# Kernel optimization log

Hardware: AMD Instinct MI355X
Metric: run time of the kernel (lower is better)

Reference implementation:

```python
import jax, jax.numpy as jnp
import numpy as np

GRID = (160, 160, 160)
RADIUS_FACTOR = 3.0
PATCH = 20      # fixed patch edge; covers ceil(c+r)-floor(c-r)+1 for r <= 9 voxels
CHUNK = 500
N_POINTS = 25000


def _quat_to_rot(q):
    # normalized quaternion -> rotation matrix (matches torch reference)
    q = q / jnp.clip(jnp.linalg.norm(q, axis=-1, keepdims=True), 1e-6)
    w, x, y, z = q[..., 0], q[..., 1], q[..., 2], q[..., 3]
    ww, xx, yy, zz = w * w, x * x, y * y, z * z
    wx, wy, wz = w * x, w * y, w * z
    xy, xz, yz = x * y, x * z, y * z
    r0 = jnp.stack([ww + xx - yy - zz, 2 * (xy - wz), 2 * (xz + wy)], -1)
    r1 = jnp.stack([2 * (xy + wz), ww - xx + yy - zz, 2 * (yz - wx)], -1)
    r2 = jnp.stack([2 * (xz - wy), 2 * (yz + wx), ww - xx - yy + zz], -1)
    return jnp.stack([r0, r1, r2], -2)


def setup_inputs():
    key = jax.random.key(0)
    k1, k2, k3, k4 = jax.random.split(key, 4)
    centers = jax.random.uniform(k1, (N_POINTS, 3), dtype=jnp.float32)
    # scales in [1.5, 3.0] voxels -> patch radius = 3*max(scale) <= 9 < PATCH/2
    log_scales = jnp.log(jax.random.uniform(k2, (N_POINTS, 3), minval=1.5, maxval=3.0, dtype=jnp.float32))
    quats = jax.random.normal(k3, (N_POINTS, 4), dtype=jnp.float32)
    rho = 0.1 * jax.random.normal(k4, (N_POINTS, 2), dtype=jnp.float32)  # (real, imag)
    return {"centers": centers, "log_scales": log_scales, "quats": quats, "rho": rho}


def _splat(centers, log_scales, quats, rho):
    D, H, W = GRID
    span = jnp.array([D - 1, H - 1, W - 1], jnp.float32)
    scales = jnp.exp(log_scales)                                  # [N,3]
    R = _quat_to_rot(quats)                                       # [N,3,3]
    inv = 1.0 / jnp.clip(scales, 1e-4) ** 2                       # diag of S^-2
    prec = jnp.einsum('nij,nj,nkj->nik', R, inv, R)               # R diag R^T, [N,3,3]
    cv = centers * span                                           # voxel-space centers
    rad = jnp.max(scales, axis=-1) * RADIUS_FACTOR                # per-point patch radius
    base = jnp.floor(cv - rad[:, None]).astype(jnp.int32)         # zmin/ymin/xmin (pre-clip)
    hi = jnp.ceil(cv + rad[:, None]).astype(jnp.int32)            # zmax/ymax/xmax (pre-clip)
    amp_mag = jnp.sqrt(rho[:, 0] ** 2 + rho[:, 1] ** 2)
    valid = (amp_mag >= 1e-6) & (rad >= 1e-3)                     # torch skip conditions
    dims = jnp.array([D, H, W], jnp.int32)

    nchunk = N_POINTS // CHUNK
    ck = lambda a: a.reshape((nchunk, CHUNK) + a.shape[1:])
    xs = (ck(cv), ck(base), ck(hi), ck(prec), ck(rho), ck(valid))
    offs = jnp.arange(PATCH, dtype=jnp.int32)

    def step(vol, x):
        cv_c, base_c, hi_c, p, rho_c, val_c = x
        idx = base_c[:, :, None] + offs                           # [C,3,P] voxel indices
        d = idx.astype(jnp.float32) - cv_c[:, :, None]            # [C,3,P] rel coords
        m = (idx >= 0) & (idx < dims[None, :, None]) & (idx <= hi_c[:, :, None])
        dz, dy, dx = d[:, 0], d[:, 1], d[:, 2]                    # [C,P] each
        # exponent = rel^T prec rel, built separably (prec is symmetric)
        e = ((p[:, 0, 0, None] * dz * dz)[:, :, None, None]
             + (p[:, 1, 1, None] * dy * dy)[:, None, :, None]
             + (p[:, 2, 2, None] * dx * dx)[:, None, None, :]
             + (2.0 * p[:, 0, 1, None, None] * dz[:, :, None] * dy[:, None, :])[:, :, :, None]
             + (2.0 * p[:, 0, 2, None, None] * dz[:, :, None] * dx[:, None, :])[:, :, None, :]
             + (2.0 * p[:, 1, 2, None, None] * dy[:, :, None] * dx[:, None, :])[:, None, :, :])
        w = jnp.exp(-0.5 * e)                                     # [C,P,P,P]
        mask = (m[:, 0, :, None, None] & m[:, 1, None, :, None] & m[:, 2, None, None, :]
                & val_c[:, None, None, None])
        w = jnp.where(mask, w, 0.0)
        iz = jnp.clip(idx[:, 0], 0, D - 1)
        iy = jnp.clip(idx[:, 1], 0, H - 1)
        ix = jnp.clip(idx[:, 2], 0, W - 1)
        lin = (iz[:, :, None, None] * H + iy[:, None, :, None]) * W + ix[:, None, None, :]
        contrib = w[..., None] * rho_c[:, None, None, None, :]    # [C,P,P,P,2] (re,im)
        vol = vol.at[lin.reshape(-1)].add(contrib.reshape(-1, 2))
        return vol, None

    vol, _ = jax.lax.scan(step, jnp.zeros((D * H * W, 2), jnp.float32), xs)
    return vol.reshape(D, H, W, 2)


def reference(centers, log_scales, quats, rho):
    return _splat(centers, log_scales, quats, rho)
```

## Files before the change

kernel.cpp:

```cpp
#include <hip/hip_runtime.h>


namespace {
constexpr int GD = 160, GH = 160, GW = 160;
constexpr int NPTS = 25000;
constexpr int PATCH = 20;
constexpr int TS  = 8;
constexpr int TPD = GD / TS;
constexpr int NT  = TPD * TPD * TPD;
constexpr int CAP = 384;
constexpr int PSTRIDE = 16;
constexpr float L2E = 1.4426950408889634f;
}


__global__ __launch_bounds__(256) void prep_bin(
    const float* __restrict__ centers,
    const float* __restrict__ log_scales,
    const float* __restrict__ quats,
    const float* __restrict__ rho,
    float* __restrict__ params,
    int* __restrict__ counts,
    unsigned short* __restrict__ list)
{
    const int t = blockIdx.x * 256 + threadIdx.x;
    const int gid  = t >> 6;
    const int lane = t & 63;

    const float r0 = rho[gid * 2 + 0];
    const float r1 = rho[gid * 2 + 1];
    const float s0 = __expf(log_scales[gid * 3 + 0]);
    const float s1 = __expf(log_scales[gid * 3 + 1]);
    const float s2 = __expf(log_scales[gid * 3 + 2]);

    const float smax = fmaxf(s0, fmaxf(s1, s2));
    const float rad  = smax * 3.0f;
    const float amp2 = r0 * r0 + r1 * r1;

    const float cvz = centers[gid * 3 + 0] * (float)(GD - 1);
    const float cvy = centers[gid * 3 + 1] * (float)(GH - 1);
    const float cvx = centers[gid * 3 + 2] * (float)(GW - 1);

    const int bz = (int)floorf(cvz - rad);
    const int by = (int)floorf(cvy - rad);
    const int bx = (int)floorf(cvx - rad);
    const int hz = (int)ceilf(cvz + rad);
    const int hy = (int)ceilf(cvy + rad);
    const int hx = (int)ceilf(cvx + rad);

    const int loz = max(bz, 0), upz = min(min(hz, GD - 1), bz + PATCH - 1);
    const int loy = max(by, 0), upy = min(min(hy, GH - 1), by + PATCH - 1);
    const int lox = max(bx, 0), upx = min(min(hx, GW - 1), bx + PATCH - 1);

    const bool valid = (amp2 >= 1e-12f) && (rad >= 1e-3f) &&
                       (upz >= loz) && (upy >= loy) && (upx >= lox);

    const float q0 = quats[gid * 4 + 0], q1 = quats[gid * 4 + 1];
    const float q2 = quats[gid * 4 + 2], q3 = quats[gid * 4 + 3];
    float qn = sqrtf(q0 * q0 + q1 * q1 + q2 * q2 + q3 * q3);
    qn = fmaxf(qn, 1e-6f);
    const float w = q0 / qn, x = q1 / qn, y = q2 / qn, z = q3 / qn;

    const float R00 = w * w + x * x - y * y - z * z;
    const float R01 = 2.f * (x * y - w * z);
    const float R02 = 2.f * (x * z + w * y);
    const float R10 = 2.f * (x * y + w * z);
    const float R11 = w * w - x * x + y * y - z * z;
    const float R12 = 2.f * (y * z - w * x);
    const float R20 = 2.f * (x * z - w * y);
    const float R21 = 2.f * (y * z + w * x);
    const float R22 = w * w - x * x - y * y + z * z;

    const float c0 = fmaxf(s0, 1e-4f); const float i0 = 1.f / (c0 * c0);
    const float c1 = fmaxf(s1, 1e-4f); const float i1 = 1.f / (c1 * c1);
    const float c2 = fmaxf(s2, 1e-4f); const float i2 = 1.f / (c2 * c2);

    const float p00 = R00 * R00 * i0 + R01 * R01 * i1 + R02 * R02 * i2;
    const float p01 = R00 * R10 * i0 + R01 * R11 * i1 + R02 * R12 * i2;
    const float p02 = R00 * R20 * i0 + R01 * R21 * i1 + R02 * R22 * i2;
    const float p11 = R10 * R10 * i0 + R11 * R11 * i1 + R12 * R12 * i2;
    const float p12 = R10 * R20 * i0 + R11 * R21 * i1 + R12 * R22 * i2;
    const float p22 = R20 * R20 * i0 + R21 * R21 * i1 + R22 * R22 * i2;

    const float q00s = -0.5f * L2E * p00;
    const float v    = __builtin_amdgcn_exp2f(2.f * q00s);

    const int zl = valid ? loz : 255, zu = valid ? upz : 0;
    const int yl = valid ? loy : 255, yu = valid ? upy : 0;
    const int xl = valid ? lox : 255, xu = valid ? upx : 0;
    const int loPack = zl | (yl << 8) | (xl << 16) | (zu << 24);
    const int upPack = yu | (xu << 8);

    if (lane == 0) {
        float4* P = reinterpret_cast<float4*>(params + (size_t)gid * PSTRIDE);
        P[0] = make_float4(q00s, -L2E * p01, -L2E * p02, -0.5f * L2E * p11);
        P[1] = make_float4(-L2E * p12, -0.5f * L2E * p22, cvz, cvy);
        P[2] = make_float4(cvx, r0, r1, __int_as_float(loPack));
        P[3] = make_float4(__int_as_float(upPack), v, 0.f, 0.f);
    }

    if (!valid) return;

    const int tz0 = loz >> 3, tz1 = upz >> 3;
    const int ty0 = loy >> 3, ty1 = upy >> 3;
    const int tx0 = lox >> 3, tx1 = upx >> 3;
    const int tz = tz0 + (lane >> 4);
    const int ty = ty0 + ((lane >> 2) & 3);
    const int tx = tx0 + (lane & 3);
    if (tz > tz1 || ty > ty1 || tx > tx1) return;
    const int tile = (tz * TPD + ty) * TPD + tx;
    const int pos = atomicAdd(&counts[tile], 1);
    if (pos < CAP) list[(size_t)tile * CAP + pos] = (unsigned short)gid;
}

__global__ __launch_bounds__(256) void gather(
    const float* __restrict__ params,
    const int* __restrict__ counts,
    const unsigned short* __restrict__ list,
    float2* __restrict__ out)
{
    const int wli  = threadIdx.x >> 6;
    const int tile = __builtin_amdgcn_readfirstlane(blockIdx.x * 4 + wli);
    const int tz = tile / (TPD * TPD);
    const int rem = tile - tz * (TPD * TPD);
    const int ty = rem / TPD;
    const int tx = rem - ty * TPD;

    const int lane = threadIdx.x & 63;
    const int ly = lane >> 3, lx = lane & 7;
    const int iy = ty * TS + ly;
    const int ix = tx * TS + lx;
    const int z0 = tz * TS;
    const float fy = (float)iy, fx = (float)ix, fz = (float)z0;

    int cnt = counts[tile];
    if (cnt > CAP) cnt = CAP;
    const float4* p4 = reinterpret_cast<const float4*>(params);
    const unsigned short* tl = list + (size_t)tile * CAP;

    float ar[8], ai[8];
#pragma unroll
    for (int i = 0; i < 8; ++i) { ar[i] = 0.f; ai[i] = 0.f; }

    for (int g = 0; g < cnt; ++g) {
        const int gid = __builtin_amdgcn_readfirstlane((int)tl[g]);
        const float4 Pa = p4[(size_t)gid * 4 + 0];
        const float4 Pb = p4[(size_t)gid * 4 + 1];
        const float4 Pc = p4[(size_t)gid * 4 + 2];
        const float4 Pd = p4[(size_t)gid * 4 + 3];
        const int lo = __float_as_int(Pc.w);
        const int up = __float_as_int(Pd.x);
        const int loy_ = (lo >> 8) & 255, lox_ = (lo >> 16) & 255;
        const int upy_ = up & 255,        upx_ = (up >> 8) & 255;
        if (iy < loy_ || iy > upy_ || ix < lox_ || ix > upx_) continue;
        const int zl = (lo & 255) - z0;
        const int zu = ((lo >> 24) & 255) - z0;

        const float dy = fy - Pb.w;
        const float dx = fx - Pc.x;
        const float C = fmaf(dy, fmaf(Pa.w, dy, Pb.x * dx), Pb.y * dx * dx);
        const float B = fmaf(Pa.y, dy, Pa.z * dx);
        const float dz = fz - Pb.z;
        const float t0 = fmaf(dz, fmaf(Pa.x, dz, B), C);
        const float dt = fmaf(Pa.x, fmaf(2.f, dz, 1.f), B);
        float wgt = __builtin_amdgcn_exp2f(t0);
        float u   = __builtin_amdgcn_exp2f(dt);
        const float v = Pd.y;
        const float r0 = Pc.y, r1 = Pc.z;
#pragma unroll
        for (int i = 0; i < 8; ++i) {
            const float wm = (i >= zl && i <= zu) ? wgt : 0.f;
            ar[i] = fmaf(wm, r0, ar[i]);
            ai[i] = fmaf(wm, r1, ai[i]);
            wgt *= u;
            u *= v;
        }
    }

#pragma unroll
    for (int i = 0; i < 8; ++i)
        out[((size_t)(z0 + i) * GH + iy) * GW + ix] = make_float2(ar[i], ai[i]);
}

extern "C" void kernel_launch(void* const* d_in, const int* in_sizes, int n_in,
                              void* d_out, int out_size, void* d_ws, size_t ws_size,
                              hipStream_t stream) {
    const float* centers    = (const float*)d_in[0];
    const float* log_scales = (const float*)d_in[1];
    const float* quats      = (const float*)d_in[2];
    const float* rho        = (const float*)d_in[3];

    float* params = (float*)d_ws;
    int* counts = (int*)(params + (size_t)NPTS * PSTRIDE);
    unsigned short* list = (unsigned short*)(counts + NT);

    hipMemsetAsync(counts, 0, NT * sizeof(int), stream);
    prep_bin<<<(NPTS * 64) / 256, 256, 0, stream>>>(centers, log_scales, quats,
                                                    rho, params, counts, list);
    gather<<<NT / 4, 256, 0, stream>>>(params, counts, list, (float2*)d_out);
}
```

Before: 191.8 us.

## Fuse memset, binning and gather into one cooperative persistent kernel

Replaces the memset plus two kernel launches with a single cooperative kernel. It zeroes the counts, computes per-point parameters and bins them serially per thread, then gathers per tile, with grid-wide syncs between phases. In the gather phase each wave stages batches of 16 point parameter records in LDS instead of issuing scalar global loads per point. Lane masking is made branchless. The aim is to remove launch gaps and per-point global load latency, at the cost of grid.sync overhead, persistent-grid occupancy limits, and serial atomic loops per point in the binning phase.

New measurement: 377.9 us. 97.0% more time.

```diff
diff --git a/kernel.cpp b/kernel.cpp
--- a/kernel.cpp
+++ b/kernel.cpp
@@ -1,4 +1,7 @@
 #include <hip/hip_runtime.h>
+#include <hip/hip_cooperative_groups.h>
+
+namespace cg = cooperative_groups;
 
 
 namespace {
@@ -14,172 +17,183 @@
 }
 
 
-__global__ __launch_bounds__(256) void prep_bin(
+__global__ __launch_bounds__(256, 8) void fused(
     const float* __restrict__ centers,
     const float* __restrict__ log_scales,
     const float* __restrict__ quats,
     const float* __restrict__ rho,
     float* __restrict__ params,
     int* __restrict__ counts,
-    unsigned short* __restrict__ list)
+    unsigned short* __restrict__ list,
+    float2* __restrict__ out)
 {
-    const int t = blockIdx.x * 256 + threadIdx.x;
-    const int gid  = t >> 6;
-    const int lane = t & 63;
-
-    const float r0 = rho[gid * 2 + 0];
-    const float r1 = rho[gid * 2 + 1];
-    const float s0 = __expf(log_scales[gid * 3 + 0]);
-    const float s1 = __expf(log_scales[gid * 3 + 1]);
-    const float s2 = __expf(log_scales[gid * 3 + 2]);
-
-    const float smax = fmaxf(s0, fmaxf(s1, s2));
-    const float rad  = smax * 3.0f;
-    const float amp2 = r0 * r0 + r1 * r1;
-
-    const float cvz = centers[gid * 3 + 0] * (float)(GD - 1);
-    const float cvy = centers[gid * 3 + 1] * (float)(GH - 1);
-    const float cvx = centers[gid * 3 + 2] * (float)(GW - 1);
-
-    const int bz = (int)floorf(cvz - rad);
-    const int by = (int)floorf(cvy - rad);
-    const int bx = (int)floorf(cvx - rad);
-    const int hz = (int)ceilf(cvz + rad);
-    const int hy = (int)ceilf(cvy + rad);
-    const int hx = (int)ceilf(cvx + rad);
-
-    const int loz = max(bz, 0), upz = min(min(hz, GD - 1), bz + PATCH - 1);
-    const int loy = max(by, 0), upy = min(min(hy, GH - 1), by + PATCH - 1);
-    const int lox = max(bx, 0), upx = min(min(hx, GW - 1), bx + PATCH - 1);
-
-    const bool valid = (amp2 >= 1e-12f) && (rad >= 1e-3f) &&
-                       (upz >= loz) && (upy >= loy) && (upx >= lox);
-
-    const float q0 = quats[gid * 4 + 0], q1 = quats[gid * 4 + 1];
-    const float q2 = quats[gid * 4 + 2], q3 = quats[gid * 4 + 3];
-    float qn = sqrtf(q0 * q0 + q1 * q1 + q2 * q2 + q3 * q3);
-    qn = fmaxf(qn, 1e-6f);
-    const float w = q0 / qn, x = q1 / qn, y = q2 / qn, z = q3 / qn;
-
-    const float R00 = w * w + x * x - y * y - z * z;
-    const float R01 = 2.f * (x * y - w * z);
-    const float R02 = 2.f * (x * z + w * y);
-    const float R10 = 2.f * (x * y + w * z);
-    const float R11 = w * w - x * x + y * y - z * z;
-    const float R12 = 2.f * (y * z - w * x);
-    const float R20 = 2.f * (x * z - w * y);
-    const float R21 = 2.f * (y * z + w * x);
-    const float R22 = w * w - x * x - y * y + z * z;
-
-    const float c0 = fmaxf(s0, 1e-4f); const float i0 = 1.f / (c0 * c0);
-    const float c1 = fmaxf(s1, 1e-4f); const float i1 = 1.f / (c1 * c1);
-    const float c2 = fmaxf(s2, 1e-4f); const float i2 = 1.f / (c2 * c2);
-
-    const float p00 = R00 * R00 * i0 + R01 * R01 * i1 + R02 * R02 * i2;
-    const float p01 = R00 * R10 * i0 + R01 * R11 * i1 + R02 * R12 * i2;
-    const float p02 = R00 * R20 * i0 + R01 * R21 * i1 + R02 * R22 * i2;
-    const float p11 = R10 * R10 * i0 + R11 * R11 * i1 + R12 * R12 * i2;
-    const float p12 = R10 * R20 * i0 + R11 * R21 * i1 + R12 * R22 * i2;
-    const float p22 = R20 * R20 * i0 + R21 * R21 * i1 + R22 * R22 * i2;
-
-    const float q00s = -0.5f * L2E * p00;
-    const float v    = __builtin_amdgcn_exp2f(2.f * q00s);
-
-    const int zl = valid ? loz : 255, zu = valid ? upz : 0;
-    const int yl = valid ? loy : 255, yu = valid ? upy : 0;
-    const int xl = valid ? lox : 255, xu = valid ? upx : 0;
-    const int loPack = zl | (yl << 8) | (xl << 16) | (zu << 24);
-    const int upPack = yu | (xu << 8);
-
-    if (lane == 0) {
+    cg::grid_group grid = cg::this_grid();
+    const int nthreads = (int)gridDim.x * 256;
+    const int tid = blockIdx.x * 256 + threadIdx.x;
+
+    for (int i = tid; i < NT; i += nthreads) counts[i] = 0;
+    grid.sync();
+
+    for (int gid = tid; gid < NPTS; gid += nthreads) {
+        const float r0 = rho[gid * 2 + 0];
+        const float r1 = rho[gid * 2 + 1];
+        const float s0 = __expf(log_scales[gid * 3 + 0]);
+        const float s1 = __expf(log_scales[gid * 3 + 1]);
+        const float s2 = __expf(log_scales[gid * 3 + 2]);
+
+        const float smax = fmaxf(s0, fmaxf(s1, s2));
+        const float rad  = smax * 3.0f;
+        const float amp2 = r0 * r0 + r1 * r1;
+
+        const float cvz = centers[gid * 3 + 0] * (float)(GD - 1);
+        const float cvy = centers[gid * 3 + 1] * (float)(GH - 1);
+        const float cvx = centers[gid * 3 + 2] * (float)(GW - 1);
+
+        const int bz = (int)floorf(cvz - rad);
+        const int by = (int)floorf(cvy - rad);
+        const int bx = (int)floorf(cvx - rad);
+        const int hz = (int)ceilf(cvz + rad);
+        const int hy = (int)ceilf(cvy + rad);
+        const int hx = (int)ceilf(cvx + rad);
+
+        const int loz = max(bz, 0), upz = min(min(hz, GD - 1), bz + PATCH - 1);
+        const int loy = max(by, 0), upy = min(min(hy, GH - 1), by + PATCH - 1);
+        const int lox = max(bx, 0), upx = min(min(hx, GW - 1), bx + PATCH - 1);
+
+        const bool valid = (amp2 >= 1e-12f) && (rad >= 1e-3f) &&
+                           (upz >= loz) && (upy >= loy) && (upx >= lox);
+
+        const float q0 = quats[gid * 4 + 0], q1 = quats[gid * 4 + 1];
+        const float q2 = quats[gid * 4 + 2], q3 = quats[gid * 4 + 3];
+        float qn = sqrtf(q0 * q0 + q1 * q1 + q2 * q2 + q3 * q3);
+        qn = fmaxf(qn, 1e-6f);
+        const float w = q0 / qn, x = q1 / qn, y = q2 / qn, z = q3 / qn;
+
+        const float R00 = w * w + x * x - y * y - z * z;
+        const float R01 = 2.f * (x * y - w * z);
+        const float R02 = 2.f * (x * z + w * y);
+        const float R10 = 2.f * (x * y + w * z);
+        const float R11 = w * w - x * x + y * y - z * z;
+        const float R12 = 2.f * (y * z - w * x);
+        const float R20 = 2.f * (x * z - w * y);
+        const float R21 = 2.f * (y * z + w * x);
+        const float R22 = w * w - x * x - y * y + z * z;
+
+        const float c0 = fmaxf(s0, 1e-4f); const float i0 = 1.f / (c0 * c0);
+        const float c1 = fmaxf(s1, 1e-4f); const float i1 = 1.f / (c1 * c1);
+        const float c2 = fmaxf(s2, 1e-4f); const float i2 = 1.f / (c2 * c2);
+
+        const float p00 = R00 * R00 * i0 + R01 * R01 * i1 + R02 * R02 * i2;
+        const float p01 = R00 * R10 * i0 + R01 * R11 * i1 + R02 * R12 * i2;
+        const float p02 = R00 * R20 * i0 + R01 * R21 * i1 + R02 * R22 * i2;
+        const float p11 = R10 * R10 * i0 + R11 * R11 * i1 + R12 * R12 * i2;
+        const float p12 = R10 * R20 * i0 + R11 * R21 * i1 + R12 * R22 * i2;
+        const float p22 = R20 * R20 * i0 + R21 * R21 * i1 + R22 * R22 * i2;
+
+        const float q00s = -0.5f * L2E * p00;
+        const float v    = __builtin_amdgcn_exp2f(2.f * q00s);
+
+        const int zl = valid ? loz : 255, zu = valid ? upz : 0;
+        const int yl = valid ? loy : 255, yu = valid ? upy : 0;
+        const int xl = valid ? lox : 255, xu = valid ? upx : 0;
+        const int loPack = zl | (yl << 8) | (xl << 16) | (zu << 24);
+        const int upPack = yu | (xu << 8);
+
         float4* P = reinterpret_cast<float4*>(params + (size_t)gid * PSTRIDE);
         P[0] = make_float4(q00s, -L2E * p01, -L2E * p02, -0.5f * L2E * p11);
         P[1] = make_float4(-L2E * p12, -0.5f * L2E * p22, cvz, cvy);
         P[2] = make_float4(cvx, r0, r1, __int_as_float(loPack));
         P[3] = make_float4(__int_as_float(upPack), v, 0.f, 0.f);
+
+        if (valid) {
+            const int tz0 = loz >> 3, tz1 = upz >> 3;
+            const int ty0 = loy >> 3, ty1 = upy >> 3;
+            const int tx0 = lox >> 3, tx1 = upx >> 3;
+            for (int tz = tz0; tz <= tz1; ++tz)
+                for (int ty = ty0; ty <= ty1; ++ty)
+                    for (int tx = tx0; tx <= tx1; ++tx) {
+                        const int t = (tz * TPD + ty) * TPD + tx;
+                        const int pos = atomicAdd(&counts[t], 1);
+                        if (pos < CAP)
+                            list[(size_t)t * CAP + pos] = (unsigned short)gid;
+                    }
+        }
     }
-
-    if (!valid) return;
-
-    const int tz0 = loz >> 3, tz1 = upz >> 3;
-    const int ty0 = loy >> 3, ty1 = upy >> 3;
-    const int tx0 = lox >> 3, tx1 = upx >> 3;
-    const int tz = tz0 + (lane >> 4);
-    const int ty = ty0 + ((lane >> 2) & 3);
-    const int tx = tx0 + (lane & 3);
-    if (tz > tz1 || ty > ty1 || tx > tx1) return;
-    const int tile = (tz * TPD + ty) * TPD + tx;
-    const int pos = atomicAdd(&counts[tile], 1);
-    if (pos < CAP) list[(size_t)tile * CAP + pos] = (unsigned short)gid;
-}
-
-__global__ __launch_bounds__(256) void gather(
-    const float* __restrict__ params,
-    const int* __restrict__ counts,
-    const unsigned short* __restrict__ list,
-    float2* __restrict__ out)
-{
+    grid.sync();
+
     const int wli  = threadIdx.x >> 6;
-    const int tile = __builtin_amdgcn_readfirstlane(blockIdx.x * 4 + wli);
-    const int tz = tile / (TPD * TPD);
-    const int rem = tile - tz * (TPD * TPD);
-    const int ty = rem / TPD;
-    const int tx = rem - ty * TPD;
-
     const int lane = threadIdx.x & 63;
     const int ly = lane >> 3, lx = lane & 7;
-    const int iy = ty * TS + ly;
-    const int ix = tx * TS + lx;
-    const int z0 = tz * TS;
-    const float fy = (float)iy, fx = (float)ix, fz = (float)z0;
-
-    int cnt = counts[tile];
-    if (cnt > CAP) cnt = CAP;
+    const int totalWaves = nthreads >> 6;
+    __shared__ float4 sP[4][16][4];
     const float4* p4 = reinterpret_cast<const float4*>(params);
-    const unsigned short* tl = list + (size_t)tile * CAP;
-
-    float ar[8], ai[8];
+
+    for (int tile = blockIdx.x * 4 + wli; tile < NT; tile += totalWaves) {
+        const int tz = tile / (TPD * TPD);
+        const int rem = tile - tz * (TPD * TPD);
+        const int ty = rem / TPD;
+        const int tx = rem - ty * TPD;
+        const int iy = ty * TS + ly;
+        const int ix = tx * TS + lx;
+        const int z0 = tz * TS;
+        const float fy = (float)iy, fx = (float)ix, fz = (float)z0;
+
+        int cnt = __builtin_amdgcn_readfirstlane(counts[tile]);
+        if (cnt > CAP) cnt = CAP;
+        const unsigned short* tl = list + (size_t)tile * CAP;
+
+        float ar[8], ai[8];
 #pragma unroll
-    for (int i = 0; i < 8; ++i) { ar[i] = 0.f; ai[i] = 0.f; }
-
-    for (int g = 0; g < cnt; ++g) {
-        const int gid = __builtin_amdgcn_readfirstlane((int)tl[g]);
-        const float4 Pa = p4[(size_t)gid * 4 + 0];
-        const float4 Pb = p4[(size_t)gid * 4 + 1];
-        const float4 Pc = p4[(size_t)gid * 4 + 2];
-        const float4 Pd = p4[(size_t)gid * 4 + 3];
-        const int lo = __float_as_int(Pc.w);
-        const int up = __float_as_int(Pd.x);
-        const int loy_ = (lo >> 8) & 255, lox_ = (lo >> 16) & 255;
-        const int upy_ = up & 255,        upx_ = (up >> 8) & 255;
-        if (iy < loy_ || iy > upy_ || ix < lox_ || ix > upx_) continue;
-        const int zl = (lo & 255) - z0;
-        const int zu = ((lo >> 24) & 255) - z0;
-
-        const float dy = fy - Pb.w;
-        const float dx = fx - Pc.x;
-        const float C = fmaf(dy, fmaf(Pa.w, dy, Pb.x * dx), Pb.y * dx * dx);
-        const float B = fmaf(Pa.y, dy, Pa.z * dx);
-        const float dz = fz - Pb.z;
-        const float t0 = fmaf(dz, fmaf(Pa.x, dz, B), C);
-        const float dt = fmaf(Pa.x, fmaf(2.f, dz, 1.f), B);
-        float wgt = __builtin_amdgcn_exp2f(t0);
-        float u   = __builtin_amdgcn_exp2f(dt);
-        const float v = Pd.y;
-        const float r0 = Pc.y, r1 = Pc.z;
+        for (int i = 0; i < 8; ++i) { ar[i] = 0.f; ai[i] = 0.f; }
+
+        for (int b0 = 0; b0 < cnt; b0 += 16) {
+            const int nb = min(16, cnt - b0);
+            const int slot = lane >> 2, word = lane & 3;
+            if (slot < nb) {
+                const int g = tl[b0 + slot];
+                sP[wli][slot][word] = p4[(size_t)g * 4 + word];
+            }
+            for (int g = 0; g < nb; ++g) {
+                const float4 Pa = sP[wli][g][0];
+                const float4 Pb = sP[wli][g][1];
+                const float4 Pc = sP[wli][g][2];
+                const float2 Pd = *reinterpret_cast<const float2*>(&sP[wli][g][3]);
+                const int lo = __builtin_amdgcn_readfirstlane(__float_as_int(Pc.w));
+                const int up = __builtin_amdgcn_readfirstlane(__float_as_int(Pd.x));
+                const int loy_ = (lo >> 8) & 255, lox_ = (lo >> 16) & 255;
+                const int upy_ = up & 255,        upx_ = (up >> 8) & 255;
+                const int zl = (lo & 255) - z0;
+                const int zu = ((lo >> 24) & 255) - z0;
+                const bool yx = (iy >= loy_) & (iy <= upy_) &
+                                (ix >= lox_) & (ix <= upx_);
+
+                const float dy = fy - Pb.w;
+                const float dx = fx - Pc.x;
+                const float C = fmaf(dy, fmaf(Pa.w, dy, Pb.x * dx), Pb.y * dx * dx);
+                const float B = fmaf(Pa.y, dy, Pa.z * dx);
+                const float dz = fz - Pb.z;
+                const float t0 = fmaf(dz, fmaf(Pa.x, dz, B), C);
+                const float dt = fmaf(Pa.x, fmaf(2.f, dz, 1.f), B);
+                float wgt = __builtin_amdgcn_exp2f(t0);
+                float u   = __builtin_amdgcn_exp2f(dt);
+                const float v = Pd.y;
+                const float r0m = yx ? Pc.y : 0.f;
+                const float r1m = yx ? Pc.z : 0.f;
 #pragma unroll
-        for (int i = 0; i < 8; ++i) {
-            const float wm = (i >= zl && i <= zu) ? wgt : 0.f;
-            ar[i] = fmaf(wm, r0, ar[i]);
-            ai[i] = fmaf(wm, r1, ai[i]);
-            wgt *= u;
-            u *= v;
+                for (int i = 0; i < 8; ++i) {
+                    const float wm = (i >= zl && i <= zu) ? wgt : 0.f;
+                    ar[i] = fmaf(wm, r0m, ar[i]);
+                    ai[i] = fmaf(wm, r1m, ai[i]);
+                    wgt *= u;
+                    u *= v;
+                }
+            }
         }
+
+#pragma unroll
+        for (int i = 0; i < 8; ++i)
+            out[((size_t)(z0 + i) * GH + iy) * GW + ix] = make_float2(ar[i], ai[i]);
     }
-
-#pragma unroll
-    for (int i = 0; i < 8; ++i)
-        out[((size_t)(z0 + i) * GH + iy) * GW + ix] = make_float2(ar[i], ai[i]);
 }
 
 extern "C" void kernel_launch(void* const* d_in, const int* in_sizes, int n_in,
@@ -193,9 +207,17 @@
     float* params = (float*)d_ws;
     int* counts = (int*)(params + (size_t)NPTS * PSTRIDE);
     unsigned short* list = (unsigned short*)(counts + NT);
-
-    hipMemsetAsync(counts, 0, NT * sizeof(int), stream);
-    prep_bin<<<(NPTS * 64) / 256, 256, 0, stream>>>(centers, log_scales, quats,
-                                                    rho, params, counts, list);
-    gather<<<NT / 4, 256, 0, stream>>>(params, counts, list, (float2*)d_out);
+    float2* out = (float2*)d_out;
+
+    int maxb = 4;
+    (void)hipOccupancyMaxActiveBlocksPerMultiprocessor(&maxb, fused, 256, 0);
+    if (maxb < 1) maxb = 1;
+    int nblk = maxb * 256;
+    if (nblk > NT / 4) nblk = NT / 4;
+
+    void* args[] = {(void*)&centers, (void*)&log_scales, (void*)&quats,
+                    (void*)&rho, (void*)&params, (void*)&counts,
+                    (void*)&list, (void*)&out};
+    hipLaunchCooperativeKernel((const void*)fused, dim3(nblk), dim3(256),
+                               args, 0, stream);
 }
```
